# Kernel optimization log

Hardware: AMD Instinct MI355X
Metric: run time of the kernel (lower is better)

The kernel has to match this reference:

```python
import jax, jax.numpy as jnp
import numpy as np

N = 100000      # num nodes
E = 800000      # num edges (avg degree 8)
D_IN = 128
D_OUT = 128
ALPHA = 0.5


def setup_inputs() -> dict:
    key = jax.random.key(0)
    ks = jax.random.split(key, 8)
    x = jax.random.normal(ks[0], (N, D_IN), dtype=jnp.float32)
    edge_index = jax.random.randint(ks[1], (2, E), 0, N, dtype=jnp.int64)
    s = 1.0 / np.sqrt(D_IN)
    # lin_self (nn.Linear), and per-direction SAGEConv lin_l (root_weight=False, bias=True)
    W_self = jax.random.uniform(ks[2], (D_IN, D_OUT), jnp.float32, -s, s)
    b_self = jax.random.uniform(ks[3], (D_OUT,), jnp.float32, -s, s)
    W_s2d = jax.random.uniform(ks[4], (D_IN, D_OUT), jnp.float32, -s, s)
    b_s2d = jnp.zeros((D_OUT,), jnp.float32)
    W_d2s = jax.random.uniform(ks[5], (D_IN, D_OUT), jnp.float32, -s, s)
    b_d2s = jnp.zeros((D_OUT,), jnp.float32)
    return {"x": x, "W_self": W_self, "b_self": b_self,
            "W_s2d": W_s2d, "b_s2d": b_s2d,
            "W_d2s": W_d2s, "b_d2s": b_d2s,
            "edge_index": edge_index}


def _mean_aggr(x, gather_idx, scatter_idx, num_nodes):
    # mean of x[gather_idx] segmented by scatter_idx; isolated nodes -> 0 (PyG scatter-mean semantics)
    summed = jax.ops.segment_sum(x[gather_idx], scatter_idx, num_segments=num_nodes)
    cnt = jax.ops.segment_sum(jnp.ones(gather_idx.shape, x.dtype), scatter_idx, num_segments=num_nodes)
    return summed / jnp.maximum(cnt, 1.0)[:, None]


def reference(x, W_self, b_self, W_s2d, b_s2d, W_d2s, b_d2s, edge_index):
    src, dst = edge_index[0], edge_index[1]
    n = x.shape[0]
    # flow='source_to_target': aggregate src features at dst (in-neighbors)
    agg_in = _mean_aggr(x, src, dst, n)
    # flow='target_to_source': aggregate dst features at src (out-neighbors)
    agg_out = _mean_aggr(x, dst, src, n)
    out = (x @ W_self + b_self
           + (1.0 - ALPHA) * (agg_in @ W_s2d + b_s2d)
           + ALPHA * (agg_out @ W_d2s + b_d2s))
    return out
```

## Files before the change

### kernel.cpp

```cpp
#include <hip/hip_runtime.h>


#define D 128
#define KTOT 384
#define NP 16
#define NPSH 4
#define RNGP 12500
#define NCH 48
#define TN 512
#define BT 512

typedef unsigned short u16;
typedef unsigned char u8;
typedef short bf16x8 __attribute__((ext_vector_type(8)));
typedef float f32x4 __attribute__((ext_vector_type(4)));
typedef float f32x2 __attribute__((ext_vector_type(2)));
typedef int i32x4 __attribute__((ext_vector_type(4)));

__device__ __forceinline__ u16 f2bf(float f) {
    unsigned u = __float_as_uint(f);
    unsigned r = (u + 0x7FFF + ((u >> 16) & 1)) >> 16;
    return (u16)r;
}

__device__ __forceinline__ unsigned cvt_pk_bf16(float a, float b) {
    unsigned r;
    asm("v_cvt_pk_bf16_f32 %0, %1, %2" : "=v"(r) : "v"(a), "v"(b));
    return r;
}

__device__ __forceinline__ void gload_lds16(const void* g, void* l) {
    __builtin_amdgcn_global_load_lds(
        (const __attribute__((address_space(1))) unsigned*)g,
        (__attribute__((address_space(3))) unsigned*)l, 16, 0, 0);
}

__global__ __launch_bounds__(256) void prep_w_k(const float* __restrict__ W0,
                                                const float* __restrict__ W1,
                                                const float* __restrict__ W2,
                                                const float* __restrict__ b0,
                                                const float* __restrict__ b1,
                                                const float* __restrict__ b2,
                                                u16* __restrict__ Wt,
                                                float* __restrict__ biasc) {
    int idx = blockIdx.x * 256 + threadIdx.x;
    if (idx < 128 * KTOT) {
        int n = idx / KTOT;
        int kt = idx - n * KTOT;
        int seg = kt >> 7;
        int k = kt & 127;
        const float* W = (seg == 0) ? W0 : (seg == 1) ? W1 : W2;
        Wt[n * KTOT + kt] = f2bf(W[k * D + n]);
    }
    if (idx < D) {
        biasc[idx] = b0[idx] + 0.5f * (b1[idx] + b2[idx]);
    }
}

__global__ __launch_bounds__(256) void conv_x_k(const float* __restrict__ x,
                                                u16* __restrict__ Ab,
                                                unsigned* __restrict__ xq,
                                                int N) {
    int gid = blockIdx.x * 256 + threadIdx.x;
    int node = gid >> 5;
    int c = gid & 31;
    if (node >= N) return;
    float4 v = *(const float4*)&x[(size_t)node * D + c * 4];
    ushort4 o;
    o.x = f2bf(v.x); o.y = f2bf(v.y); o.z = f2bf(v.z); o.w = f2bf(v.w);
    *(ushort4*)&Ab[(size_t)node * KTOT + c * 4] = o;
    int q = __builtin_amdgcn_cvt_pk_fp8_f32(v.x, v.y, 0, false);
    q = __builtin_amdgcn_cvt_pk_fp8_f32(v.z, v.w, q, true);
    xq[(size_t)node * 32 + c] = (unsigned)q;
}

__global__ __launch_bounds__(BT) void count_part_k(const int* __restrict__ ei,
                                                   int E, int N, int n2, int S2,
                                                   u8* __restrict__ deg2) {
    __shared__ unsigned cnt[RNGP / 4];
    const int p = blockIdx.x & (NP - 1);
    const int c = blockIdx.x >> NPSH;
    const int lo = p * RNGP;
    const int hi = min(n2, lo + RNGP);
    for (int i = threadIdx.x; i < RNGP / 4; i += BT) cnt[i] = 0;
    __syncthreads();

    const int pc = (((E + NCH - 1) / NCH) + 3) & ~3;
    const int beg = c * pc;
    const int end = min(E, beg + pc);
    for (int e = beg + ((int)threadIdx.x << 2); e < end; e += BT * 4) {
        if (e + 3 < end) {
            i32x4 s4 = __builtin_nontemporal_load((const i32x4*)&ei[e]);
            i32x4 d4 = __builtin_nontemporal_load((const i32x4*)&ei[E + e]);
#pragma unroll
            for (int j = 0; j < 4; ++j) {
                int d = d4[j];
                if (d >= lo && d < hi) {
                    int i = d - lo;
                    atomicAdd(&cnt[i >> 2], 1u << (8 * (i & 3)));
                }
                int os = N + s4[j];
                if (os >= lo && os < hi) {
                    int i = os - lo;
                    atomicAdd(&cnt[i >> 2], 1u << (8 * (i & 3)));
                }
            }
        } else {
            for (int j = 0; j < end - e; ++j) {
                int s = ei[e + j], d = ei[E + e + j];
                if (d >= lo && d < hi) {
                    int i = d - lo;
                    atomicAdd(&cnt[i >> 2], 1u << (8 * (i & 3)));
                }
                int os = N + s;
                if (os >= lo && os < hi) {
                    int i = os - lo;
                    atomicAdd(&cnt[i >> 2], 1u << (8 * (i & 3)));
                }
            }
        }
    }
    __syncthreads();
    unsigned* dst = (unsigned*)(deg2 + (size_t)c * S2 + lo);
    const int spanw = (hi - lo) >> 2;
    for (int i = threadIdx.x; i < spanw; i += BT) dst[i] = cnt[i];
}

__global__ __launch_bounds__(256) void rowscan_k(u8* __restrict__ deg2,
                                                 int* __restrict__ deg,
                                                 int n2, int S2) {
    __shared__ u8 t[NCH][TN];
    const int base = blockIdx.x * TN;
#pragma unroll
    for (int c = 0; c < NCH; ++c) {
        unsigned* src = (unsigned*)&deg2[(size_t)c * S2 + base];
        unsigned* dl = (unsigned*)&t[c][0];
        for (int i = threadIdx.x; i < TN / 4; i += 256) dl[i] = src[i];
    }
    __syncthreads();
    for (int j = threadIdx.x; j < TN; j += 256) {
        int run = 0;
#pragma unroll
        for (int c = 0; c < NCH; ++c) {
            int v = t[c][j];
            t[c][j] = (u8)run;
            run += v;
        }
        if (base + j < n2) deg[base + j] = run;
    }
    __syncthreads();
#pragma unroll
    for (int c = 0; c < NCH; ++c) {
        unsigned* dstg = (unsigned*)&deg2[(size_t)c * S2 + base];
        unsigned* sl = (unsigned*)&t[c][0];
        for (int i = threadIdx.x; i < TN / 4; i += 256) dstg[i] = sl[i];
    }
}

__device__ __forceinline__ int block_incl_scan(int v, int* wsum) {
    int lane = threadIdx.x & 63;
    int wv = threadIdx.x >> 6;
#pragma unroll
    for (int off = 1; off < 64; off <<= 1) {
        int t = __shfl_up(v, off, 64);
        if (lane >= off) v += t;
    }
    if (lane == 63) wsum[wv] = v;
    __syncthreads();
    int add = 0;
    for (int w = 0; w < wv; ++w) add += wsum[w];
    return v + add;
}

__global__ __launch_bounds__(256) void scan1_k(const int* __restrict__ in, int n,
                                               int* __restrict__ bsum) {
    __shared__ int wsum[4];
    int i = blockIdx.x * 256 + threadIdx.x;
    int v = (i < n) ? in[i] : 0;
    int s = block_incl_scan(v, wsum);
    if (threadIdx.x == 255) bsum[blockIdx.x] = s;
}

__global__ __launch_bounds__(1024) void scan2_k(int* __restrict__ bsum, int nb) {
    __shared__ int wsum[16];
    int i = threadIdx.x;
    int v = (i < nb) ? bsum[i] : 0;
    int s = block_incl_scan(v, wsum);
    if (i < nb) bsum[i] = s - v;
}

__global__ __launch_bounds__(256) void scan3_k(const int* __restrict__ in, int n,
                                               const int* __restrict__ bsum,
                                               int* __restrict__ ptr) {
    __shared__ int wsum[4];
    int i = blockIdx.x * 256 + threadIdx.x;
    int v = (i < n) ? in[i] : 0;
    int s = block_incl_scan(v, wsum);
    int off = bsum[blockIdx.x];
    if (i < n) ptr[i] = off + s - v;
    if (i == n - 1) ptr[n] = off + s;
}

__global__ __launch_bounds__(BT) void fill2_part_k(const int* __restrict__ ei,
                                                   int E, int N, int n2, int S2,
                                                   const int* __restrict__ ptr,
                                                   const u8* __restrict__ deg2,
                                                   int* __restrict__ adj) {
    __shared__ unsigned cnt[RNGP / 4];
    const int p = blockIdx.x & (NP - 1);
    const int c = blockIdx.x >> NPSH;
    const int lo = p * RNGP;
    const int hi = min(n2, lo + RNGP);
    const unsigned* d2w = (const unsigned*)(deg2 + (size_t)c * S2 + lo);
    for (int i = threadIdx.x; i < RNGP / 4; i += BT) cnt[i] = d2w[i];
    __syncthreads();

    const int pc = (((E + NCH - 1) / NCH) + 3) & ~3;
    const int beg = c * pc;
    const int end = min(E, beg + pc);
    for (int e = beg + ((int)threadIdx.x << 2); e < end; e += BT * 4) {
        if (e + 3 < end) {
            i32x4 s4 = __builtin_nontemporal_load((const i32x4*)&ei[e]);
            i32x4 d4 = __builtin_nontemporal_load((const i32x4*)&ei[E + e]);
#pragma unroll
            for (int j = 0; j < 4; ++j) {
                int s = s4[j], d = d4[j];
                if (d >= lo && d < hi) {
                    int i = d - lo;
                    unsigned old = atomicAdd(&cnt[i >> 2], 1u << (8 * (i & 3)));
                    int off = (int)((old >> (8 * (i & 3))) & 0xFFu);
                    adj[ptr[d] + off] = s;
                }
                int os = N + s;
                if (os >= lo && os < hi) {
                    int i = os - lo;
                    unsigned old = atomicAdd(&cnt[i >> 2], 1u << (8 * (i & 3)));
                    int off = (int)((old >> (8 * (i & 3))) & 0xFFu);
                    adj[ptr[os] + off] = d;
                }
            }
        } else {
            for (int j = 0; j < end - e; ++j) {
                int s = ei[e + j], d = ei[E + e + j];
                if (d >= lo && d < hi) {
                    int i = d - lo;
                    unsigned old = atomicAdd(&cnt[i >> 2], 1u << (8 * (i & 3)));
                    int off = (int)((old >> (8 * (i & 3))) & 0xFFu);
                    adj[ptr[d] + off] = s;
                }
                int os = N + s;
                if (os >= lo && os < hi) {
                    int i = os - lo;
                    unsigned old = atomicAdd(&cnt[i >> 2], 1u << (8 * (i & 3)));
                    int off = (int)((old >> (8 * (i & 3))) & 0xFFu);
                    adj[ptr[os] + off] = d;
                }
            }
        }
    }
}

__global__ __launch_bounds__(256) void agg_k(const unsigned* __restrict__ xq,
                                             u16* __restrict__ Ab,
                                             const int* __restrict__ ptr,
                                             const int* __restrict__ adj,
                                             int N) {
    int gid = blockIdx.x * 256 + threadIdx.x;
    int node = gid >> 3;
    int l8 = gid & 7;
    if (node >= N) return;
    const int dir = blockIdx.y;
    const int ci = dir * N + node;

    int beg = ptr[ci], end = ptr[ci + 1];
    f32x2 acc[8];
#pragma unroll
    for (int j = 0; j < 8; ++j) acc[j] = (f32x2){0.f, 0.f};

    for (int j0 = beg; j0 < end; j0 += 8) {
        int a = (j0 + l8 < end) ? adj[j0 + l8] : 0;
        int m = min(8, end - j0);
        for (int t = 0; t < m; ++t) {
            int nbr = __shfl(a, t, 8);
            uint4 q = *(const uint4*)((const char*)xq + ((size_t)nbr * 128 + l8 * 16));
            acc[0] += __builtin_amdgcn_cvt_pk_f32_fp8((int)q.x, false);
            acc[1] += __builtin_amdgcn_cvt_pk_f32_fp8((int)q.x, true);
            acc[2] += __builtin_amdgcn_cvt_pk_f32_fp8((int)q.y, false);
            acc[3] += __builtin_amdgcn_cvt_pk_f32_fp8((int)q.y, true);
            acc[4] += __builtin_amdgcn_cvt_pk_f32_fp8((int)q.z, false);
            acc[5] += __builtin_amdgcn_cvt_pk_f32_fp8((int)q.z, true);
            acc[6] += __builtin_amdgcn_cvt_pk_f32_fp8((int)q.w, false);
            acc[7] += __builtin_amdgcn_cvt_pk_f32_fp8((int)q.w, true);
        }
    }

    float s = 0.5f / fmaxf((float)(end - beg), 1.0f);
    unsigned w[8];
#pragma unroll
    for (int j = 0; j < 8; ++j)
        w[j] = cvt_pk_bf16(acc[j].x * s, acc[j].y * s);
    u16* dst = &Ab[(size_t)node * KTOT + 128 + dir * 128 + l8 * 16];
    *(uint4*)dst = make_uint4(w[0], w[1], w[2], w[3]);
    *(uint4*)(dst + 8) = make_uint4(w[4], w[5], w[6], w[7]);
}

#define BK 64
__global__ __launch_bounds__(256) void gemm_k(const u16* __restrict__ Ab,
                                              const u16* __restrict__ Wt,
                                              const float* __restrict__ biasc,
                                              float* __restrict__ out, int N) {
    __shared__ u16 As[128 * BK];
    __shared__ u16 Bs[128 * BK];

    const int tid = threadIdx.x;
    const int row0 = blockIdx.x * 128;
    const int w = tid >> 6;
    const int lane = tid & 63;
    const int m = lane & 15;
    const int quad = lane >> 4;
    const int wr = w >> 1;
    const int wc = w & 1;

    f32x4 acc[4][4];
#pragma unroll
    for (int i = 0; i < 4; ++i)
#pragma unroll
        for (int j = 0; j < 4; ++j) acc[i][j] = (f32x4){0.f, 0.f, 0.f, 0.f};

    for (int kb = 0; kb < KTOT / BK; ++kb) {
        const int k0 = kb * BK;
        __syncthreads();
#pragma unroll
        for (int i = 0; i < 4; ++i) {
            int ci = i * 256 + tid;
            int r = ci >> 3;
            int q8 = ci & 7;
            gload_lds16(&Ab[(size_t)(row0 + r) * KTOT + k0 + q8 * 8],
                        &As[(i * 256 + w * 64) * 8]);
        }
#pragma unroll
        for (int i = 0; i < 4; ++i) {
            int ci = i * 256 + tid;
            int n = ci >> 3;
            int q8 = ci & 7;
            gload_lds16(&Wt[(size_t)n * KTOT + k0 + q8 * 8],
                        &Bs[(i * 256 + w * 64) * 8]);
        }
        __syncthreads();

        bf16x8 a[4][2], b[4][2];
#pragma unroll
        for (int i = 0; i < 4; ++i)
#pragma unroll
            for (int s = 0; s < 2; ++s)
                a[i][s] = *(const bf16x8*)&As[(wr * 64 + i * 16 + m) * BK + s * 32 + quad * 8];
#pragma unroll
        for (int j = 0; j < 4; ++j)
#pragma unroll
            for (int s = 0; s < 2; ++s)
                b[j][s] = *(const bf16x8*)&Bs[(wc * 64 + j * 16 + m) * BK + s * 32 + quad * 8];
#pragma unroll
        for (int i = 0; i < 4; ++i)
#pragma unroll
            for (int j = 0; j < 4; ++j) {
                acc[i][j] = __builtin_amdgcn_mfma_f32_16x16x32_bf16(a[i][0], b[j][0], acc[i][j], 0, 0, 0);
                acc[i][j] = __builtin_amdgcn_mfma_f32_16x16x32_bf16(a[i][1], b[j][1], acc[i][j], 0, 0, 0);
            }
    }

#pragma unroll
    for (int j = 0; j < 4; ++j) {
        int col = wc * 64 + j * 16 + m;
        float bv = biasc[col];
#pragma unroll
        for (int i = 0; i < 4; ++i) {
            int rbase = row0 + wr * 64 + i * 16 + quad * 4;
#pragma unroll
            for (int r = 0; r < 4; ++r) {
                int row = rbase + r;
                if (row < N) out[(size_t)row * D + col] = acc[i][j][r] + bv;
            }
        }
    }
}


extern "C" void kernel_launch(void* const* d_in, const int* in_sizes, int n_in,
                              void* d_out, int out_size, void* d_ws, size_t ws_size,
                              hipStream_t stream) {
    const float* x      = (const float*)d_in[0];
    const float* W_self = (const float*)d_in[1];
    const float* b_self = (const float*)d_in[2];
    const float* W_s2d  = (const float*)d_in[3];
    const float* b_s2d  = (const float*)d_in[4];
    const float* W_d2s  = (const float*)d_in[5];
    const float* b_d2s  = (const float*)d_in[6];
    const int*   ei     = (const int*)d_in[7];

    const int N = in_sizes[0] / D;
    const int E = in_sizes[7] / 2;
    float* out = (float*)d_out;
    char* ws = (char*)d_ws;

    const int n2 = 2 * N;
    const int S2 = ((n2 + TN - 1) / TN) * TN;

    size_t o = 0;
    u16* Ab = (u16*)(ws + o);        o += (size_t)N * KTOT * sizeof(u16);
    unsigned* xq = (unsigned*)(ws + o); o += (size_t)N * 32 * sizeof(unsigned);
    u16* Wt = (u16*)(ws + o);        o += (size_t)D * KTOT * sizeof(u16);
    float* biasc = (float*)(ws + o); o += D * sizeof(float);
    int* deg = (int*)(ws + o);       o += (size_t)n2 * sizeof(int);
    int* ptr = (int*)(ws + o);       o += ((size_t)n2 + 1) * sizeof(int);
    u8* deg2 = (u8*)(ws + o);        o += (size_t)NCH * S2 * sizeof(u8);
    int* adj = (int*)(ws + o);       o += (size_t)2 * E * sizeof(int);
    int* bs  = (int*)(ws + o);       o += 1024 * sizeof(int);

    const int nb2 = (n2 + 255) / 256;
    const int node32_blocks = (int)(((size_t)N * 32 + 255) / 256);
    const int node8_blocks = (int)(((size_t)N * 8 + 255) / 256);
    const int gemm_blocks = (N + 127) / 128;
    const int cs_grid = NCH * NP;
    const int rs_grid = S2 / TN;

    prep_w_k<<<(128 * KTOT + 255) / 256, 256, 0, stream>>>(W_self, W_s2d, W_d2s,
                                                           b_self, b_s2d, b_d2s,
                                                           Wt, biasc);
    conv_x_k<<<node32_blocks, 256, 0, stream>>>(x, Ab, xq, N);

    count_part_k<<<cs_grid, BT, 0, stream>>>(ei, E, N, n2, S2, deg2);
    rowscan_k<<<rs_grid, 256, 0, stream>>>(deg2, deg, n2, S2);
    scan1_k<<<nb2, 256, 0, stream>>>(deg, n2, bs);
    scan2_k<<<1, 1024, 0, stream>>>(bs, nb2);
    scan3_k<<<nb2, 256, 0, stream>>>(deg, n2, bs, ptr);
    fill2_part_k<<<cs_grid, BT, 0, stream>>>(ei, E, N, n2, S2, ptr, deg2, adj);

    dim3 agrid(node8_blocks, 2);
    agg_k<<<agrid, 256, 0, stream>>>(xq, Ab, ptr, adj, N);

    gemm_k<<<gemm_blocks, 256, 0, stream>>>(Ab, Wt, biasc, out, N);
}
```

Measured before the change: 256.8 us.

## Fuse preprocessing kernels, fold scan block-sums into rowscan, unroll gather by two

Merges weight prep, x conversion and edge counting into one launch that dispatches on block index. It also moves the per-tile degree sum into rowscan so the separate scan1 pass goes away. Scan3 now uses 512-thread blocks that match the rowscan tiles. The aggregation loop issues two neighbor loads per iteration to expose more memory parallelism. Together these cut launch count and let independent preprocessing overlap, but the count blocks drop from 512 to 256 threads, so each count block runs longer.

```diff
diff --git a/kernel.cpp b/kernel.cpp
--- a/kernel.cpp
+++ b/kernel.cpp
@@ -35,101 +35,95 @@
         (__attribute__((address_space(3))) unsigned*)l, 16, 0, 0);
 }
 
-__global__ __launch_bounds__(256) void prep_w_k(const float* __restrict__ W0,
-                                                const float* __restrict__ W1,
-                                                const float* __restrict__ W2,
-                                                const float* __restrict__ b0,
-                                                const float* __restrict__ b1,
-                                                const float* __restrict__ b2,
-                                                u16* __restrict__ Wt,
-                                                float* __restrict__ biasc) {
-    int idx = blockIdx.x * 256 + threadIdx.x;
-    if (idx < 128 * KTOT) {
-        int n = idx / KTOT;
-        int kt = idx - n * KTOT;
-        int seg = kt >> 7;
-        int k = kt & 127;
-        const float* W = (seg == 0) ? W0 : (seg == 1) ? W1 : W2;
-        Wt[n * KTOT + kt] = f2bf(W[k * D + n]);
-    }
-    if (idx < D) {
-        biasc[idx] = b0[idx] + 0.5f * (b1[idx] + b2[idx]);
-    }
-}
-
-__global__ __launch_bounds__(256) void conv_x_k(const float* __restrict__ x,
-                                                u16* __restrict__ Ab,
-                                                unsigned* __restrict__ xq,
-                                                int N) {
-    int gid = blockIdx.x * 256 + threadIdx.x;
-    int node = gid >> 5;
-    int c = gid & 31;
-    if (node >= N) return;
-    float4 v = *(const float4*)&x[(size_t)node * D + c * 4];
-    ushort4 o;
-    o.x = f2bf(v.x); o.y = f2bf(v.y); o.z = f2bf(v.z); o.w = f2bf(v.w);
-    *(ushort4*)&Ab[(size_t)node * KTOT + c * 4] = o;
-    int q = __builtin_amdgcn_cvt_pk_fp8_f32(v.x, v.y, 0, false);
-    q = __builtin_amdgcn_cvt_pk_fp8_f32(v.z, v.w, q, true);
-    xq[(size_t)node * 32 + c] = (unsigned)q;
-}
-
-__global__ __launch_bounds__(BT) void count_part_k(const int* __restrict__ ei,
-                                                   int E, int N, int n2, int S2,
-                                                   u8* __restrict__ deg2) {
+__global__ __launch_bounds__(256) void fused_pcc_k(
+    const int* __restrict__ ei, u8* __restrict__ deg2,
+    const float* __restrict__ x, u16* __restrict__ Ab, unsigned* __restrict__ xq,
+    const float* __restrict__ W0, const float* __restrict__ W1,
+    const float* __restrict__ W2, const float* __restrict__ b0,
+    const float* __restrict__ b1, const float* __restrict__ b2,
+    u16* __restrict__ Wt, float* __restrict__ biasc,
+    int N, int E, int n2, int S2, int convB) {
     __shared__ unsigned cnt[RNGP / 4];
-    const int p = blockIdx.x & (NP - 1);
-    const int c = blockIdx.x >> NPSH;
-    const int lo = p * RNGP;
-    const int hi = min(n2, lo + RNGP);
-    for (int i = threadIdx.x; i < RNGP / 4; i += BT) cnt[i] = 0;
-    __syncthreads();
-
-    const int pc = (((E + NCH - 1) / NCH) + 3) & ~3;
-    const int beg = c * pc;
-    const int end = min(E, beg + pc);
-    for (int e = beg + ((int)threadIdx.x << 2); e < end; e += BT * 4) {
-        if (e + 3 < end) {
-            i32x4 s4 = __builtin_nontemporal_load((const i32x4*)&ei[e]);
-            i32x4 d4 = __builtin_nontemporal_load((const i32x4*)&ei[E + e]);
-#pragma unroll
-            for (int j = 0; j < 4; ++j) {
-                int d = d4[j];
-                if (d >= lo && d < hi) {
-                    int i = d - lo;
-                    atomicAdd(&cnt[i >> 2], 1u << (8 * (i & 3)));
-                }
-                int os = N + s4[j];
-                if (os >= lo && os < hi) {
-                    int i = os - lo;
-                    atomicAdd(&cnt[i >> 2], 1u << (8 * (i & 3)));
+    const int bx = (int)blockIdx.x;
+    const int tid = threadIdx.x;
+    if (bx < NCH * NP) {
+        const int p = bx & (NP - 1);
+        const int c = bx >> NPSH;
+        const int lo = p * RNGP;
+        const int hi = min(n2, lo + RNGP);
+        for (int i = tid; i < RNGP / 4; i += 256) cnt[i] = 0;
+        __syncthreads();
+        const int pc = (((E + NCH - 1) / NCH) + 3) & ~3;
+        const int beg = c * pc;
+        const int end = min(E, beg + pc);
+        for (int e = beg + (tid << 2); e < end; e += 256 * 4) {
+            if (e + 3 < end) {
+                i32x4 s4 = __builtin_nontemporal_load((const i32x4*)&ei[e]);
+                i32x4 d4 = __builtin_nontemporal_load((const i32x4*)&ei[E + e]);
+#pragma unroll
+                for (int j = 0; j < 4; ++j) {
+                    int d = d4[j];
+                    if (d >= lo && d < hi) {
+                        int i = d - lo;
+                        atomicAdd(&cnt[i >> 2], 1u << (8 * (i & 3)));
+                    }
+                    int os = N + s4[j];
+                    if (os >= lo && os < hi) {
+                        int i = os - lo;
+                        atomicAdd(&cnt[i >> 2], 1u << (8 * (i & 3)));
+                    }
+                }
+            } else {
+                for (int j = 0; j < end - e; ++j) {
+                    int s = ei[e + j], d = ei[E + e + j];
+                    if (d >= lo && d < hi) {
+                        int i = d - lo;
+                        atomicAdd(&cnt[i >> 2], 1u << (8 * (i & 3)));
+                    }
+                    int os = N + s;
+                    if (os >= lo && os < hi) {
+                        int i = os - lo;
+                        atomicAdd(&cnt[i >> 2], 1u << (8 * (i & 3)));
+                    }
                 }
             }
-        } else {
-            for (int j = 0; j < end - e; ++j) {
-                int s = ei[e + j], d = ei[E + e + j];
-                if (d >= lo && d < hi) {
-                    int i = d - lo;
-                    atomicAdd(&cnt[i >> 2], 1u << (8 * (i & 3)));
-                }
-                int os = N + s;
-                if (os >= lo && os < hi) {
-                    int i = os - lo;
-                    atomicAdd(&cnt[i >> 2], 1u << (8 * (i & 3)));
-                }
-            }
-        }
-    }
-    __syncthreads();
-    unsigned* dst = (unsigned*)(deg2 + (size_t)c * S2 + lo);
-    const int spanw = (hi - lo) >> 2;
-    for (int i = threadIdx.x; i < spanw; i += BT) dst[i] = cnt[i];
+        }
+        __syncthreads();
+        unsigned* dst = (unsigned*)(deg2 + (size_t)c * S2 + lo);
+        const int spanw = (hi - lo) >> 2;
+        for (int i = tid; i < spanw; i += 256) dst[i] = cnt[i];
+    } else if (bx < NCH * NP + convB) {
+        int gid = (bx - NCH * NP) * 256 + tid;
+        int node = gid >> 5;
+        int c = gid & 31;
+        if (node >= N) return;
+        float4 v = *(const float4*)&x[(size_t)node * D + c * 4];
+        ushort4 o;
+        o.x = f2bf(v.x); o.y = f2bf(v.y); o.z = f2bf(v.z); o.w = f2bf(v.w);
+        *(ushort4*)&Ab[(size_t)node * KTOT + c * 4] = o;
+        int q = __builtin_amdgcn_cvt_pk_fp8_f32(v.x, v.y, 0, false);
+        q = __builtin_amdgcn_cvt_pk_fp8_f32(v.z, v.w, q, true);
+        xq[(size_t)node * 32 + c] = (unsigned)q;
+    } else {
+        int idx = (bx - NCH * NP - convB) * 256 + tid;
+        if (idx < 128 * KTOT) {
+            int n = idx / KTOT;
+            int kt = idx - n * KTOT;
+            int seg = kt >> 7;
+            int k = kt & 127;
+            const float* W = (seg == 0) ? W0 : (seg == 1) ? W1 : W2;
+            Wt[n * KTOT + kt] = f2bf(W[k * D + n]);
+        }
+        if (idx < D) biasc[idx] = b0[idx] + 0.5f * (b1[idx] + b2[idx]);
+    }
 }
 
 __global__ __launch_bounds__(256) void rowscan_k(u8* __restrict__ deg2,
                                                  int* __restrict__ deg,
+                                                 int* __restrict__ tsum,
                                                  int n2, int S2) {
     __shared__ u8 t[NCH][TN];
+    __shared__ int red[256];
     const int base = blockIdx.x * TN;
 #pragma unroll
     for (int c = 0; c < NCH; ++c) {
@@ -138,6 +132,7 @@
         for (int i = threadIdx.x; i < TN / 4; i += 256) dl[i] = src[i];
     }
     __syncthreads();
+    int part = 0;
     for (int j = threadIdx.x; j < TN; j += 256) {
         int run = 0;
 #pragma unroll
@@ -146,9 +141,18 @@
             t[c][j] = (u8)run;
             run += v;
         }
-        if (base + j < n2) deg[base + j] = run;
-    }
+        if (base + j < n2) {
+            deg[base + j] = run;
+            part += run;
+        }
+    }
+    red[threadIdx.x] = part;
     __syncthreads();
+    for (int off = 128; off > 0; off >>= 1) {
+        if ((int)threadIdx.x < off) red[threadIdx.x] += red[threadIdx.x + off];
+        __syncthreads();
+    }
+    if (threadIdx.x == 0) tsum[blockIdx.x] = red[0];
 #pragma unroll
     for (int c = 0; c < NCH; ++c) {
         unsigned* dstg = (unsigned*)&deg2[(size_t)c * S2 + base];
@@ -170,15 +174,6 @@
     int add = 0;
     for (int w = 0; w < wv; ++w) add += wsum[w];
     return v + add;
-}
-
-__global__ __launch_bounds__(256) void scan1_k(const int* __restrict__ in, int n,
-                                               int* __restrict__ bsum) {
-    __shared__ int wsum[4];
-    int i = blockIdx.x * 256 + threadIdx.x;
-    int v = (i < n) ? in[i] : 0;
-    int s = block_incl_scan(v, wsum);
-    if (threadIdx.x == 255) bsum[blockIdx.x] = s;
 }
 
 __global__ __launch_bounds__(1024) void scan2_k(int* __restrict__ bsum, int nb) {
@@ -189,16 +184,16 @@
     if (i < nb) bsum[i] = s - v;
 }
 
-__global__ __launch_bounds__(256) void scan3_k(const int* __restrict__ in, int n,
-                                               const int* __restrict__ bsum,
+__global__ __launch_bounds__(512) void scan3_k(const int* __restrict__ deg, int n2,
+                                               const int* __restrict__ tsum,
                                                int* __restrict__ ptr) {
-    __shared__ int wsum[4];
-    int i = blockIdx.x * 256 + threadIdx.x;
-    int v = (i < n) ? in[i] : 0;
+    __shared__ int wsum[8];
+    int i = blockIdx.x * TN + threadIdx.x;
+    int v = (i < n2) ? deg[i] : 0;
     int s = block_incl_scan(v, wsum);
-    int off = bsum[blockIdx.x];
-    if (i < n) ptr[i] = off + s - v;
-    if (i == n - 1) ptr[n] = off + s;
+    int off = tsum[blockIdx.x];
+    if (i < n2) ptr[i] = off + s - v;
+    if (i == n2 - 1) ptr[n2] = off + s;
 }
 
 __global__ __launch_bounds__(BT) void fill2_part_k(const int* __restrict__ ei,
@@ -260,6 +255,18 @@
     }
 }
 
+#define ACC8(q)                                                      \
+    do {                                                             \
+        acc[0] += __builtin_amdgcn_cvt_pk_f32_fp8((int)(q).x, false);\
+        acc[1] += __builtin_amdgcn_cvt_pk_f32_fp8((int)(q).x, true); \
+        acc[2] += __builtin_amdgcn_cvt_pk_f32_fp8((int)(q).y, false);\
+        acc[3] += __builtin_amdgcn_cvt_pk_f32_fp8((int)(q).y, true); \
+        acc[4] += __builtin_amdgcn_cvt_pk_f32_fp8((int)(q).z, false);\
+        acc[5] += __builtin_amdgcn_cvt_pk_f32_fp8((int)(q).z, true); \
+        acc[6] += __builtin_amdgcn_cvt_pk_f32_fp8((int)(q).w, false);\
+        acc[7] += __builtin_amdgcn_cvt_pk_f32_fp8((int)(q).w, true); \
+    } while (0)
+
 __global__ __launch_bounds__(256) void agg_k(const unsigned* __restrict__ xq,
                                              u16* __restrict__ Ab,
                                              const int* __restrict__ ptr,
@@ -277,20 +284,23 @@
 #pragma unroll
     for (int j = 0; j < 8; ++j) acc[j] = (f32x2){0.f, 0.f};
 
+    const char* xb = (const char*)xq;
     for (int j0 = beg; j0 < end; j0 += 8) {
         int a = (j0 + l8 < end) ? adj[j0 + l8] : 0;
         int m = min(8, end - j0);
-        for (int t = 0; t < m; ++t) {
-            int nbr = __shfl(a, t, 8);
-            uint4 q = *(const uint4*)((const char*)xq + ((size_t)nbr * 128 + l8 * 16));
-            acc[0] += __builtin_amdgcn_cvt_pk_f32_fp8((int)q.x, false);
-            acc[1] += __builtin_amdgcn_cvt_pk_f32_fp8((int)q.x, true);
-            acc[2] += __builtin_amdgcn_cvt_pk_f32_fp8((int)q.y, false);
-            acc[3] += __builtin_amdgcn_cvt_pk_f32_fp8((int)q.y, true);
-            acc[4] += __builtin_amdgcn_cvt_pk_f32_fp8((int)q.z, false);
-            acc[5] += __builtin_amdgcn_cvt_pk_f32_fp8((int)q.z, true);
-            acc[6] += __builtin_amdgcn_cvt_pk_f32_fp8((int)q.w, false);
-            acc[7] += __builtin_amdgcn_cvt_pk_f32_fp8((int)q.w, true);
+        int t = 0;
+        for (; t + 2 <= m; t += 2) {
+            int n0 = __shfl(a, t, 8);
+            int n1 = __shfl(a, t + 1, 8);
+            uint4 q0 = *(const uint4*)(xb + ((size_t)n0 * 128 + l8 * 16));
+            uint4 q1 = *(const uint4*)(xb + ((size_t)n1 * 128 + l8 * 16));
+            ACC8(q0);
+            ACC8(q1);
+        }
+        if (t < m) {
+            int n0 = __shfl(a, t, 8);
+            uint4 q0 = *(const uint4*)(xb + ((size_t)n0 * 128 + l8 * 16));
+            ACC8(q0);
         }
     }
 
@@ -414,25 +424,23 @@
     int* ptr = (int*)(ws + o);       o += ((size_t)n2 + 1) * sizeof(int);
     u8* deg2 = (u8*)(ws + o);        o += (size_t)NCH * S2 * sizeof(u8);
     int* adj = (int*)(ws + o);       o += (size_t)2 * E * sizeof(int);
-    int* bs  = (int*)(ws + o);       o += 1024 * sizeof(int);
-
-    const int nb2 = (n2 + 255) / 256;
+    int* tsum = (int*)(ws + o);      o += 1024 * sizeof(int);
+
     const int node32_blocks = (int)(((size_t)N * 32 + 255) / 256);
     const int node8_blocks = (int)(((size_t)N * 8 + 255) / 256);
     const int gemm_blocks = (N + 127) / 128;
     const int cs_grid = NCH * NP;
+    const int pw_blocks = (128 * KTOT + 255) / 256;
     const int rs_grid = S2 / TN;
 
-    prep_w_k<<<(128 * KTOT + 255) / 256, 256, 0, stream>>>(W_self, W_s2d, W_d2s,
-                                                           b_self, b_s2d, b_d2s,
-                                                           Wt, biasc);
-    conv_x_k<<<node32_blocks, 256, 0, stream>>>(x, Ab, xq, N);
-
-    count_part_k<<<cs_grid, BT, 0, stream>>>(ei, E, N, n2, S2, deg2);
-    rowscan_k<<<rs_grid, 256, 0, stream>>>(deg2, deg, n2, S2);
-    scan1_k<<<nb2, 256, 0, stream>>>(deg, n2, bs);
-    scan2_k<<<1, 1024, 0, stream>>>(bs, nb2);
-    scan3_k<<<nb2, 256, 0, stream>>>(deg, n2, bs, ptr);
+    fused_pcc_k<<<cs_grid + node32_blocks + pw_blocks, 256, 0, stream>>>(
+        ei, deg2, x, Ab, xq, W_self, W_s2d, W_d2s, b_self, b_s2d, b_d2s,
+        Wt, biasc, N, E, n2, S2, node32_blocks);
+
+    rowscan_k<<<rs_grid, 256, 0, stream>>>(deg2, deg, tsum, n2, S2);
+    scan2_k<<<1, 1024, 0, stream>>>(tsum, rs_grid);
+    scan3_k<<<rs_grid, TN, 0, stream>>>(deg, n2, tsum, ptr);
+
     fill2_part_k<<<cs_grid, BT, 0, stream>>>(ei, E, N, n2, S2, ptr, deg2, adj);
 
     dim3 agrid(node8_blocks, 2);
```

Measured after the change: 251.9 us. Within noise of the previous version (-1.9%).
